# Performance work log

Measured on AMD Instinct MI355X. Metric: run time of the kernel, lower is better.

## Reference

```python
import jax, jax.numpy as jnp
import numpy as np

EMBED = 8      # embed_dim channels of 32-blade multivectors
HIDDEN = 32    # hidden_dim channels
BLADES = 32    # 2^5 Clifford blades
DT = 0.01


def setup_inputs() -> dict:
    key = jax.random.key(0)
    ks = jax.random.split(key, 8)
    B, S, N, D = 32, 256, 16, 6
    scale = lambda k, shape: jax.random.normal(k, shape, jnp.float32) * 0.1
    return {
        "x": jax.random.normal(ks[0], (B, S, N, D), jnp.float32),
        # input_proj: Linear(6, embed_dim*32)
        "W_in": scale(ks[1], (D, EMBED * BLADES)),
        "b_in": jnp.zeros((EMBED * BLADES,), jnp.float32),
        # VersorLinear(embed, hidden): channel-mixing weight shared across blades, per-blade bias
        "W1": scale(ks[2], (HIDDEN, EMBED)),
        "b1": scale(ks[3], (HIDDEN, BLADES)),
        "W2": scale(ks[4], (HIDDEN, HIDDEN)),
        "b2": scale(ks[5], (HIDDEN, BLADES)),
        "W3": scale(ks[6], (1, HIDDEN)),
        "b3": scale(ks[7], (1, BLADES)),
    }


def _versor_linear(h, W, b):
    # h: [..., in_ch, 32 blades]; mix channels, shared over blades
    return jnp.einsum('...ik,oi->...ok', h, W) + b


def _versor_act(h):
    # gate each multivector channel by sigmoid of its scalar (blade-0) part
    return h * jax.nn.sigmoid(h[..., 0:1])


def _energy(x_flat, W_in, b_in, W1, b1, W2, b2, W3, b3):
    BS, N, D = x_flat.shape
    h = x_flat @ W_in + b_in                    # [BS, N, EMBED*32]
    h = h.reshape(BS, N, EMBED, BLADES)         # [BS, N, embed, 32]
    h = _versor_act(_versor_linear(h, W1, b1))
    h = _versor_act(_versor_linear(h, W2, b2))
    h = _versor_linear(h, W3, b3)               # [BS, N, 1, 32]
    return h[..., 0].sum()                      # scalar energy


def reference(x, W_in, b_in, W1, b1, W2, b2, W3, b3):
    B, S, N, D = x.shape
    x_flat = x.reshape(B * S, N, D)
    # symplectic gradient of the Hamiltonian w.r.t. state
    grads = jax.grad(_energy)(x_flat, W_in, b_in, W1, b1, W2, b2, W3, b3)
    dq_dt = grads[..., 3:]
    dp_dt = -grads[..., :3]
    next_state = x_flat + jnp.concatenate([dq_dt, dp_dt], axis=-1) * DT
    return next_state.reshape(B, S, N, D)
```

## Files before the change

### kernel.cpp

```cpp
#include <hip/hip_runtime.h>
#include <hip/hip_bf16.h>

#define DT_STEP 0.01f

typedef __bf16 bf16x8 __attribute__((ext_vector_type(8)));
typedef float  f32x4  __attribute__((ext_vector_type(4)));

#define OFF_W2   0
#define OFF_W1   4096
#define OFF_WIND 5120
#define OFF_BIND 5312
#define OFF_B1D  5344
#define OFF_B2D  5472
#define OFF_W3   5600
#define OFF_WE   5728
#define OFF_BE   6496
#define OFF_WCP  6624
#define OFF_WAVE 7680
#define LDS_TOTAL (7680 + 4*768)

__global__ __launch_bounds__(256) void hvnn_fused(
    const float* __restrict__ x,
    const float* __restrict__ Win, const float* __restrict__ bin,
    const float* __restrict__ W1,  const float* __restrict__ b1,
    const float* __restrict__ W2,  const float* __restrict__ b2,
    const float* __restrict__ W3,
    float* __restrict__ out, int ntiles)
{
    __shared__ __align__(16) char lds[LDS_TOTAL];
    const int tid = threadIdx.x;
    const int lane = tid & 63, wv = tid >> 6;
    const int l15 = lane & 15, lhi = lane >> 4;
    const int wid = blockIdx.x * 4 + wv;
    const int nwaves = gridDim.x * 4;

    ((float4*)(lds + OFF_W2))[tid] = ((const float4*)W2)[tid];
    ((float*)(lds + OFF_W1))[tid]  = W1[tid];
    if (tid < 48) ((float*)(lds + OFF_WIND))[tid] = Win[(tid >> 3) * 256 + (tid & 7) * 32];
    if (tid < 8)  ((float*)(lds + OFF_BIND))[tid] = bin[tid * 32];
    if (tid < 32) ((float*)(lds + OFF_B1D))[tid]  = b1[tid * 32];
    if (tid < 32) ((float*)(lds + OFF_B2D))[tid]  = b2[tid * 32];
    if (tid < 32) ((float*)(lds + OFF_W3))[tid]   = W3[tid];
    __syncthreads();

    const float* W1s  = (const float*)(lds + OFF_W1);
    const float* Wind = (const float*)(lds + OFF_WIND);
    if (tid < 192) {
        int d = tid >> 5, o = tid & 31;
        float a = 0.f;
#pragma unroll
        for (int i = 0; i < 8; ++i) a = fmaf(Wind[d * 8 + i], W1s[o * 8 + i], a);
        ((float*)(lds + OFF_WE))[d * 32 + o] = a;
    }
    if (tid < 32) {
        float a = ((const float*)(lds + OFF_B1D))[tid];
#pragma unroll
        for (int i = 0; i < 8; ++i) a = fmaf(((const float*)(lds + OFF_BIND))[i], W1s[tid * 8 + i], a);
        ((float*)(lds + OFF_BE))[tid] = a;
    }
    {
        int o = tid >> 3, d = tid & 7;
        float v = 0.f;
        if (d < 6) {
            int dd = d < 3 ? d + 3 : d - 3;
            float sg = d < 3 ? DT_STEP : -DT_STEP;
            float a = 0.f;
#pragma unroll
            for (int i = 0; i < 8; ++i) a = fmaf(W1s[o * 8 + i], Wind[dd * 8 + i], a);
            v = sg * a;
        }
        ((float*)(lds + OFF_WCP))[o * 8 + d] = v;
    }
    __syncthreads();

    const float* WeS  = (const float*)(lds + OFF_WE);
    const float* W2s  = (const float*)(lds + OFF_W2);
    const float* WcpS = (const float*)(lds + OFF_WCP);
    const float* beS  = (const float*)(lds + OFF_BE);
    const float* b2dS = (const float*)(lds + OFF_B2D);
    const float* w3S  = (const float*)(lds + OFF_W3);
    const int c1 = ((l15 >> 2) << 3) | (l15 & 3);
    const int c2 = c1 + 4;

    bf16x8 awe1 = {}, awe2 = {};
    if (lhi == 0) {
#pragma unroll
        for (int d = 0; d < 6; ++d) {
            awe1[d] = (__bf16)WeS[d * 32 + c1];
            awe2[d] = (__bf16)WeS[d * 32 + c2];
        }
    }
    bf16x8 aw2f1, aw2f2, aw2b1, aw2b2;
#pragma unroll
    for (int j = 0; j < 8; ++j) {
        aw2f1[j] = (__bf16)W2s[c1 * 32 + lhi * 8 + j];
        aw2f2[j] = (__bf16)W2s[c2 * 32 + lhi * 8 + j];
        aw2b1[j] = (__bf16)W2s[(lhi * 8 + j) * 32 + c1];
        aw2b2[j] = (__bf16)W2s[(lhi * 8 + j) * 32 + c2];
    }
    bf16x8 awc = {};
    if (l15 < 6) {
#pragma unroll
        for (int j = 0; j < 8; ++j) awc[j] = (__bf16)WcpS[(lhi * 8 + j) * 8 + l15];
    }
    const f32x4 beC1 = *(const f32x4*)(beS + lhi * 8);
    const f32x4 beC2 = *(const f32x4*)(beS + lhi * 8 + 4);
    const f32x4 b2C1 = *(const f32x4*)(b2dS + lhi * 8);
    const f32x4 b2C2 = *(const f32x4*)(b2dS + lhi * 8 + 4);
    const f32x4 w3A  = *(const f32x4*)(w3S + lhi * 8);
    const f32x4 w3B  = *(const f32x4*)(w3S + lhi * 8 + 4);

    char* obufA = lds + OFF_WAVE + wv * 768;
    char* obufB = obufA + 384;
    const f32x4 z = {0.f, 0.f, 0.f, 0.f};

    auto chain = [&](bool vA, bool vB, int tA, int tB,
                     float2 xa0, float2 xa1, float2 xa2,
                     float2 xb0, float2 xb1, float2 xb2) {
        bf16x8 bxA = {}, bxB = {};
        if (lhi == 0) {
            bxA[0] = (__bf16)xa0.x; bxA[1] = (__bf16)xa0.y; bxA[2] = (__bf16)xa1.x;
            bxA[3] = (__bf16)xa1.y; bxA[4] = (__bf16)xa2.x; bxA[5] = (__bf16)xa2.y;
            bxB[0] = (__bf16)xb0.x; bxB[1] = (__bf16)xb0.y; bxB[2] = (__bf16)xb1.x;
            bxB[3] = (__bf16)xb1.y; bxB[4] = (__bf16)xb2.x; bxB[5] = (__bf16)xb2.y;
        }
        f32x4 h1A1 = __builtin_amdgcn_mfma_f32_16x16x32_bf16(awe1, bxA, beC1, 0, 0, 0);
        f32x4 h1A2 = __builtin_amdgcn_mfma_f32_16x16x32_bf16(awe2, bxA, beC2, 0, 0, 0);
        f32x4 h1B1 = __builtin_amdgcn_mfma_f32_16x16x32_bf16(awe1, bxB, beC1, 0, 0, 0);
        f32x4 h1B2 = __builtin_amdgcn_mfma_f32_16x16x32_bf16(awe2, bxB, beC2, 0, 0, 0);
        bf16x8 h1fA, h1fB; float t1A1[4], t1A2[4], t1B1[4], t1B2[4];
#pragma unroll
        for (int e = 0; e < 4; ++e) {
            float a, g;
            a = h1A1[e]; g = 1.f / (1.f + __expf(-a));
            t1A1[e] = g * fmaf(a, 1.f - g, 1.f); h1fA[e] = (__bf16)(a * g);
            a = h1A2[e]; g = 1.f / (1.f + __expf(-a));
            t1A2[e] = g * fmaf(a, 1.f - g, 1.f); h1fA[e + 4] = (__bf16)(a * g);
            a = h1B1[e]; g = 1.f / (1.f + __expf(-a));
            t1B1[e] = g * fmaf(a, 1.f - g, 1.f); h1fB[e] = (__bf16)(a * g);
            a = h1B2[e]; g = 1.f / (1.f + __expf(-a));
            t1B2[e] = g * fmaf(a, 1.f - g, 1.f); h1fB[e + 4] = (__bf16)(a * g);
        }
        f32x4 h2A1 = __builtin_amdgcn_mfma_f32_16x16x32_bf16(aw2f1, h1fA, b2C1, 0, 0, 0);
        f32x4 h2A2 = __builtin_amdgcn_mfma_f32_16x16x32_bf16(aw2f2, h1fA, b2C2, 0, 0, 0);
        f32x4 h2B1 = __builtin_amdgcn_mfma_f32_16x16x32_bf16(aw2f1, h1fB, b2C1, 0, 0, 0);
        f32x4 h2B2 = __builtin_amdgcn_mfma_f32_16x16x32_bf16(aw2f2, h1fB, b2C2, 0, 0, 0);
        bf16x8 d2fA, d2fB;
#pragma unroll
        for (int e = 0; e < 4; ++e) {
            float a, g;
            a = h2A1[e]; g = 1.f / (1.f + __expf(-a));
            d2fA[e]     = (__bf16)(w3A[e] * g * fmaf(a, 1.f - g, 1.f));
            a = h2A2[e]; g = 1.f / (1.f + __expf(-a));
            d2fA[e + 4] = (__bf16)(w3B[e] * g * fmaf(a, 1.f - g, 1.f));
            a = h2B1[e]; g = 1.f / (1.f + __expf(-a));
            d2fB[e]     = (__bf16)(w3A[e] * g * fmaf(a, 1.f - g, 1.f));
            a = h2B2[e]; g = 1.f / (1.f + __expf(-a));
            d2fB[e + 4] = (__bf16)(w3B[e] * g * fmaf(a, 1.f - g, 1.f));
        }
        f32x4 u1A1 = __builtin_amdgcn_mfma_f32_16x16x32_bf16(aw2b1, d2fA, z, 0, 0, 0);
        f32x4 u1A2 = __builtin_amdgcn_mfma_f32_16x16x32_bf16(aw2b2, d2fA, z, 0, 0, 0);
        f32x4 u1B1 = __builtin_amdgcn_mfma_f32_16x16x32_bf16(aw2b1, d2fB, z, 0, 0, 0);
        f32x4 u1B2 = __builtin_amdgcn_mfma_f32_16x16x32_bf16(aw2b2, d2fB, z, 0, 0, 0);
        bf16x8 d1fA, d1fB;
#pragma unroll
        for (int e = 0; e < 4; ++e) {
            d1fA[e]     = (__bf16)(u1A1[e] * t1A1[e]);
            d1fA[e + 4] = (__bf16)(u1A2[e] * t1A2[e]);
            d1fB[e]     = (__bf16)(u1B1[e] * t1B1[e]);
            d1fB[e + 4] = (__bf16)(u1B2[e] * t1B2[e]);
        }
        f32x4 gxA = __builtin_amdgcn_mfma_f32_16x16x32_bf16(awc, d1fA, z, 0, 0, 0);
        f32x4 gxB = __builtin_amdgcn_mfma_f32_16x16x32_bf16(awc, d1fB, z, 0, 0, 0);

        if (lhi < 2) {
#pragma unroll
            for (int e = 0; e < 4; ++e) {
                int d = lhi * 4 + e;
                if (d < 6) {
                    *(float*)(obufA + l15 * 24 + d * 4) = gxA[e];
                    *(float*)(obufB + l15 * 24 + d * 4) = gxB[e];
                }
            }
        }
        if (lane < 48) {
            if (vA) {
                float2 xv = ((const float2*)x)[(size_t)tA * 48 + lane];
                float2 g2 = *(const float2*)(obufA + lane * 8);
                ((float2*)out)[(size_t)tA * 48 + lane] = make_float2(xv.x + g2.x, xv.y + g2.y);
            }
            if (vB) {
                float2 xv = ((const float2*)x)[(size_t)tB * 48 + lane];
                float2 g2 = *(const float2*)(obufB + lane * 8);
                ((float2*)out)[(size_t)tB * 48 + lane] = make_float2(xv.x + g2.x, xv.y + g2.y);
            }
        }
    };

    const int p0 = wid, p1 = nwaves + wid;
    const int tA0 = 2 * p0, tB0 = 2 * p0 + 1, tA1 = 2 * p1, tB1 = 2 * p1 + 1;
    const bool vA0 = tA0 < ntiles, vB0 = tB0 < ntiles;
    const bool vA1 = tA1 < ntiles, vB1 = tB1 < ntiles;

    float2 a00 = {}, a01 = {}, a02 = {}, b00 = {}, b01 = {}, b02 = {};
    float2 a10 = {}, a11 = {}, a12 = {}, b10 = {}, b11 = {}, b12 = {};
    if (lhi == 0) {
        const float2* xf2 = (const float2*)x;
        if (vA0) { const float2* p = xf2 + (size_t)tA0 * 48 + l15 * 3; a00 = p[0]; a01 = p[1]; a02 = p[2]; }
        if (vB0) { const float2* p = xf2 + (size_t)tB0 * 48 + l15 * 3; b00 = p[0]; b01 = p[1]; b02 = p[2]; }
        if (vA1) { const float2* p = xf2 + (size_t)tA1 * 48 + l15 * 3; a10 = p[0]; a11 = p[1]; a12 = p[2]; }
        if (vB1) { const float2* p = xf2 + (size_t)tB1 * 48 + l15 * 3; b10 = p[0]; b11 = p[1]; b12 = p[2]; }
    }
    chain(vA0, vB0, tA0, tB0, a00, a01, a02, b00, b01, b02);
    chain(vA1, vB1, tA1, tB1, a10, a11, a12, b10, b11, b12);
}

extern "C" void kernel_launch(void* const* d_in, const int* in_sizes, int n_in,
                              void* d_out, int out_size, void* d_ws, size_t ws_size,
                              hipStream_t stream) {
    const float* x    = (const float*)d_in[0];
    const float* W_in = (const float*)d_in[1];
    const float* b_in = (const float*)d_in[2];
    const float* W1   = (const float*)d_in[3];
    const float* b1   = (const float*)d_in[4];
    const float* W2   = (const float*)d_in[5];
    const float* b2   = (const float*)d_in[6];
    const float* W3   = (const float*)d_in[7];
    float* out = (float*)d_out;

    const int NS     = in_sizes[0] / 6;
    const int ntiles = (NS + 15) / 16;
    const int blocks = (ntiles + 15) / 16;

    hvnn_fused<<<blocks, 256, 0, stream>>>(x, W_in, b_in, W1, b1, W2, b2, W3, out, ntiles);
}
```

Measured before the change: 15.38 us.

## Halve per-wave work, double grid, prefetch x early, pre-pack bf16 weights in LDS

Each wave now processes one pair of tiles instead of two, and the grid is doubled to match. This raises parallelism and shortens the serial chain each wave runs. x loads, including the residual values used in the final add, are issued at kernel start so they overlap the LDS weight setup. W2 is stored in LDS as bf16 in both row and column order, and the output projection as transposed bf16, so MFMA operands load as single vector reads instead of per-element gathers and conversions. The trade-off is twice as many blocks, each repeating the weight-setup prologue.

After: 13.72 us. 10.8% less time.

```diff
diff --git a/kernel.cpp b/kernel.cpp
--- a/kernel.cpp
+++ b/kernel.cpp
@@ -4,9 +4,11 @@
 #define DT_STEP 0.01f
 
 typedef __bf16 bf16x8 __attribute__((ext_vector_type(8)));
+typedef __bf16 bf16x4 __attribute__((ext_vector_type(4)));
 typedef float  f32x4  __attribute__((ext_vector_type(4)));
 
-#define OFF_W2   0
+#define OFF_W2R  0
+#define OFF_W2C  2048
 #define OFF_W1   4096
 #define OFF_WIND 5120
 #define OFF_BIND 5312
@@ -15,9 +17,9 @@
 #define OFF_W3   5600
 #define OFF_WE   5728
 #define OFF_BE   6496
-#define OFF_WCP  6624
-#define OFF_WAVE 7680
-#define LDS_TOTAL (7680 + 4*768)
+#define OFF_WCPT 6624
+#define OFF_WAVE 7168
+#define LDS_TOTAL (7168 + 4*768)
 
 __global__ __launch_bounds__(256) void hvnn_fused(
     const float* __restrict__ x,
@@ -32,10 +34,33 @@
     const int lane = tid & 63, wv = tid >> 6;
     const int l15 = lane & 15, lhi = lane >> 4;
     const int wid = blockIdx.x * 4 + wv;
-    const int nwaves = gridDim.x * 4;
-
-    ((float4*)(lds + OFF_W2))[tid] = ((const float4*)W2)[tid];
-    ((float*)(lds + OFF_W1))[tid]  = W1[tid];
+    const int tA = wid * 2, tB = tA + 1;
+    const bool vA = tA < ntiles, vB = tB < ntiles;
+
+    float2 xa0 = {}, xa1 = {}, xa2 = {}, xb0 = {}, xb1 = {}, xb2 = {};
+    float2 xsA = {}, xsB = {};
+    if (lhi == 0) {
+        const float2* xf2 = (const float2*)x;
+        if (vA) { const float2* p = xf2 + (size_t)tA * 48 + l15 * 3; xa0 = p[0]; xa1 = p[1]; xa2 = p[2]; }
+        if (vB) { const float2* p = xf2 + (size_t)tB * 48 + l15 * 3; xb0 = p[0]; xb1 = p[1]; xb2 = p[2]; }
+    }
+    if (lane < 48) {
+        if (vA) xsA = ((const float2*)x)[(size_t)tA * 48 + lane];
+        if (vB) xsB = ((const float2*)x)[(size_t)tB * 48 + lane];
+    }
+
+    {
+        float4 w4 = ((const float4*)W2)[tid];
+        int r = tid >> 3, c0 = (tid & 7) * 4;
+        bf16x4 b4 = { (__bf16)w4.x, (__bf16)w4.y, (__bf16)w4.z, (__bf16)w4.w };
+        *(bf16x4*)(lds + OFF_W2R + (r * 32 + c0) * 2) = b4;
+        __bf16* col = (__bf16*)(lds + OFF_W2C);
+        col[(c0 + 0) * 32 + r] = b4[0];
+        col[(c0 + 1) * 32 + r] = b4[1];
+        col[(c0 + 2) * 32 + r] = b4[2];
+        col[(c0 + 3) * 32 + r] = b4[3];
+    }
+    ((float*)(lds + OFF_W1))[tid] = W1[tid];
     if (tid < 48) ((float*)(lds + OFF_WIND))[tid] = Win[(tid >> 3) * 256 + (tid & 7) * 32];
     if (tid < 8)  ((float*)(lds + OFF_BIND))[tid] = bin[tid * 32];
     if (tid < 32) ((float*)(lds + OFF_B1D))[tid]  = b1[tid * 32];
@@ -60,28 +85,27 @@
     }
     {
         int o = tid >> 3, d = tid & 7;
-        float v = 0.f;
         if (d < 6) {
             int dd = d < 3 ? d + 3 : d - 3;
             float sg = d < 3 ? DT_STEP : -DT_STEP;
             float a = 0.f;
 #pragma unroll
             for (int i = 0; i < 8; ++i) a = fmaf(W1s[o * 8 + i], Wind[dd * 8 + i], a);
-            v = sg * a;
-        }
-        ((float*)(lds + OFF_WCP))[o * 8 + d] = v;
+            ((__bf16*)(lds + OFF_WCPT))[d * 32 + o] = (__bf16)(sg * a);
+        }
     }
     __syncthreads();
 
-    const float* WeS  = (const float*)(lds + OFF_WE);
-    const float* W2s  = (const float*)(lds + OFF_W2);
-    const float* WcpS = (const float*)(lds + OFF_WCP);
-    const float* beS  = (const float*)(lds + OFF_BE);
-    const float* b2dS = (const float*)(lds + OFF_B2D);
-    const float* w3S  = (const float*)(lds + OFF_W3);
     const int c1 = ((l15 >> 2) << 3) | (l15 & 3);
     const int c2 = c1 + 4;
-
+    const bf16x8 aw2f1 = *(const bf16x8*)(lds + OFF_W2R + (c1 * 32 + lhi * 8) * 2);
+    const bf16x8 aw2f2 = *(const bf16x8*)(lds + OFF_W2R + (c2 * 32 + lhi * 8) * 2);
+    const bf16x8 aw2b1 = *(const bf16x8*)(lds + OFF_W2C + (c1 * 32 + lhi * 8) * 2);
+    const bf16x8 aw2b2 = *(const bf16x8*)(lds + OFF_W2C + (c2 * 32 + lhi * 8) * 2);
+    bf16x8 awc = {};
+    if (l15 < 6) awc = *(const bf16x8*)(lds + OFF_WCPT + l15 * 64 + lhi * 16);
+
+    const float* WeS = (const float*)(lds + OFF_WE);
     bf16x8 awe1 = {}, awe2 = {};
     if (lhi == 0) {
 #pragma unroll
@@ -90,129 +114,100 @@
             awe2[d] = (__bf16)WeS[d * 32 + c2];
         }
     }
-    bf16x8 aw2f1, aw2f2, aw2b1, aw2b2;
-#pragma unroll
-    for (int j = 0; j < 8; ++j) {
-        aw2f1[j] = (__bf16)W2s[c1 * 32 + lhi * 8 + j];
-        aw2f2[j] = (__bf16)W2s[c2 * 32 + lhi * 8 + j];
-        aw2b1[j] = (__bf16)W2s[(lhi * 8 + j) * 32 + c1];
-        aw2b2[j] = (__bf16)W2s[(lhi * 8 + j) * 32 + c2];
-    }
-    bf16x8 awc = {};
-    if (l15 < 6) {
-#pragma unroll
-        for (int j = 0; j < 8; ++j) awc[j] = (__bf16)WcpS[(lhi * 8 + j) * 8 + l15];
-    }
-    const f32x4 beC1 = *(const f32x4*)(beS + lhi * 8);
-    const f32x4 beC2 = *(const f32x4*)(beS + lhi * 8 + 4);
-    const f32x4 b2C1 = *(const f32x4*)(b2dS + lhi * 8);
-    const f32x4 b2C2 = *(const f32x4*)(b2dS + lhi * 8 + 4);
-    const f32x4 w3A  = *(const f32x4*)(w3S + lhi * 8);
-    const f32x4 w3B  = *(const f32x4*)(w3S + lhi * 8 + 4);
+    const f32x4 beC1 = *(const f32x4*)((const float*)(lds + OFF_BE) + lhi * 8);
+    const f32x4 beC2 = *(const f32x4*)((const float*)(lds + OFF_BE) + lhi * 8 + 4);
+    const f32x4 b2C1 = *(const f32x4*)((const float*)(lds + OFF_B2D) + lhi * 8);
+    const f32x4 b2C2 = *(const f32x4*)((const float*)(lds + OFF_B2D) + lhi * 8 + 4);
+    const f32x4 w3A  = *(const f32x4*)((const float*)(lds + OFF_W3) + lhi * 8);
+    const f32x4 w3B  = *(const f32x4*)((const float*)(lds + OFF_W3) + lhi * 8 + 4);
 
     char* obufA = lds + OFF_WAVE + wv * 768;
     char* obufB = obufA + 384;
     const f32x4 z = {0.f, 0.f, 0.f, 0.f};
 
-    auto chain = [&](bool vA, bool vB, int tA, int tB,
-                     float2 xa0, float2 xa1, float2 xa2,
-                     float2 xb0, float2 xb1, float2 xb2) {
-        bf16x8 bxA = {}, bxB = {};
-        if (lhi == 0) {
-            bxA[0] = (__bf16)xa0.x; bxA[1] = (__bf16)xa0.y; bxA[2] = (__bf16)xa1.x;
-            bxA[3] = (__bf16)xa1.y; bxA[4] = (__bf16)xa2.x; bxA[5] = (__bf16)xa2.y;
-            bxB[0] = (__bf16)xb0.x; bxB[1] = (__bf16)xb0.y; bxB[2] = (__bf16)xb1.x;
-            bxB[3] = (__bf16)xb1.y; bxB[4] = (__bf16)xb2.x; bxB[5] = (__bf16)xb2.y;
-        }
-        f32x4 h1A1 = __builtin_amdgcn_mfma_f32_16x16x32_bf16(awe1, bxA, beC1, 0, 0, 0);
-        f32x4 h1A2 = __builtin_amdgcn_mfma_f32_16x16x32_bf16(awe2, bxA, beC2, 0, 0, 0);
-        f32x4 h1B1 = __builtin_amdgcn_mfma_f32_16x16x32_bf16(awe1, bxB, beC1, 0, 0, 0);
-        f32x4 h1B2 = __builtin_amdgcn_mfma_f32_16x16x32_bf16(awe2, bxB, beC2, 0, 0, 0);
-        bf16x8 h1fA, h1fB; float t1A1[4], t1A2[4], t1B1[4], t1B2[4];
+    bf16x8 bxA = {}, bxB = {};
+    if (lhi == 0) {
+        bxA[0] = (__bf16)xa0.x; bxA[1] = (__bf16)xa0.y; bxA[2] = (__bf16)xa1.x;
+        bxA[3] = (__bf16)xa1.y; bxA[4] = (__bf16)xa2.x; bxA[5] = (__bf16)xa2.y;
+        bxB[0] = (__bf16)xb0.x; bxB[1] = (__bf16)xb0.y; bxB[2] = (__bf16)xb1.x;
+        bxB[3] = (__bf16)xb1.y; bxB[4] = (__bf16)xb2.x; bxB[5] = (__bf16)xb2.y;
+    }
+
+    f32x4 h1A1 = __builtin_amdgcn_mfma_f32_16x16x32_bf16(awe1, bxA, beC1, 0, 0, 0);
+    f32x4 h1A2 = __builtin_amdgcn_mfma_f32_16x16x32_bf16(awe2, bxA, beC2, 0, 0, 0);
+    f32x4 h1B1 = __builtin_amdgcn_mfma_f32_16x16x32_bf16(awe1, bxB, beC1, 0, 0, 0);
+    f32x4 h1B2 = __builtin_amdgcn_mfma_f32_16x16x32_bf16(awe2, bxB, beC2, 0, 0, 0);
+
+    bf16x8 h1fA, h1fB; float t1A1[4], t1A2[4], t1B1[4], t1B2[4];
+#pragma unroll
+    for (int e = 0; e < 4; ++e) {
+        float a, g;
+        a = h1A1[e]; g = 1.f / (1.f + __expf(-a));
+        t1A1[e] = g * fmaf(a, 1.f - g, 1.f); h1fA[e] = (__bf16)(a * g);
+        a = h1A2[e]; g = 1.f / (1.f + __expf(-a));
+        t1A2[e] = g * fmaf(a, 1.f - g, 1.f); h1fA[e + 4] = (__bf16)(a * g);
+        a = h1B1[e]; g = 1.f / (1.f + __expf(-a));
+        t1B1[e] = g * fmaf(a, 1.f - g, 1.f); h1fB[e] = (__bf16)(a * g);
+        a = h1B2[e]; g = 1.f / (1.f + __expf(-a));
+        t1B2[e] = g * fmaf(a, 1.f - g, 1.f); h1fB[e + 4] = (__bf16)(a * g);
+    }
+
+    f32x4 h2A1 = __builtin_amdgcn_mfma_f32_16x16x32_bf16(aw2f1, h1fA, b2C1, 0, 0, 0);
+    f32x4 h2A2 = __builtin_amdgcn_mfma_f32_16x16x32_bf16(aw2f2, h1fA, b2C2, 0, 0, 0);
+    f32x4 h2B1 = __builtin_amdgcn_mfma_f32_16x16x32_bf16(aw2f1, h1fB, b2C1, 0, 0, 0);
+    f32x4 h2B2 = __builtin_amdgcn_mfma_f32_16x16x32_bf16(aw2f2, h1fB, b2C2, 0, 0, 0);
+
+    bf16x8 d2fA, d2fB;
+#pragma unroll
+    for (int e = 0; e < 4; ++e) {
+        float a, g;
+        a = h2A1[e]; g = 1.f / (1.f + __expf(-a));
+        d2fA[e]     = (__bf16)(w3A[e] * g * fmaf(a, 1.f - g, 1.f));
+        a = h2A2[e]; g = 1.f / (1.f + __expf(-a));
+        d2fA[e + 4] = (__bf16)(w3B[e] * g * fmaf(a, 1.f - g, 1.f));
+        a = h2B1[e]; g = 1.f / (1.f + __expf(-a));
+        d2fB[e]     = (__bf16)(w3A[e] * g * fmaf(a, 1.f - g, 1.f));
+        a = h2B2[e]; g = 1.f / (1.f + __expf(-a));
+        d2fB[e + 4] = (__bf16)(w3B[e] * g * fmaf(a, 1.f - g, 1.f));
+    }
+
+    f32x4 u1A1 = __builtin_amdgcn_mfma_f32_16x16x32_bf16(aw2b1, d2fA, z, 0, 0, 0);
+    f32x4 u1A2 = __builtin_amdgcn_mfma_f32_16x16x32_bf16(aw2b2, d2fA, z, 0, 0, 0);
+    f32x4 u1B1 = __builtin_amdgcn_mfma_f32_16x16x32_bf16(aw2b1, d2fB, z, 0, 0, 0);
+    f32x4 u1B2 = __builtin_amdgcn_mfma_f32_16x16x32_bf16(aw2b2, d2fB, z, 0, 0, 0);
+
+    bf16x8 d1fA, d1fB;
+#pragma unroll
+    for (int e = 0; e < 4; ++e) {
+        d1fA[e]     = (__bf16)(u1A1[e] * t1A1[e]);
+        d1fA[e + 4] = (__bf16)(u1A2[e] * t1A2[e]);
+        d1fB[e]     = (__bf16)(u1B1[e] * t1B1[e]);
+        d1fB[e + 4] = (__bf16)(u1B2[e] * t1B2[e]);
+    }
+
+    f32x4 gxA = __builtin_amdgcn_mfma_f32_16x16x32_bf16(awc, d1fA, z, 0, 0, 0);
+    f32x4 gxB = __builtin_amdgcn_mfma_f32_16x16x32_bf16(awc, d1fB, z, 0, 0, 0);
+
+    if (lhi < 2) {
 #pragma unroll
         for (int e = 0; e < 4; ++e) {
-            float a, g;
-            a = h1A1[e]; g = 1.f / (1.f + __expf(-a));
-            t1A1[e] = g * fmaf(a, 1.f - g, 1.f); h1fA[e] = (__bf16)(a * g);
-            a = h1A2[e]; g = 1.f / (1.f + __expf(-a));
-            t1A2[e] = g * fmaf(a, 1.f - g, 1.f); h1fA[e + 4] = (__bf16)(a * g);
-            a = h1B1[e]; g = 1.f / (1.f + __expf(-a));
-            t1B1[e] = g * fmaf(a, 1.f - g, 1.f); h1fB[e] = (__bf16)(a * g);
-            a = h1B2[e]; g = 1.f / (1.f + __expf(-a));
-            t1B2[e] = g * fmaf(a, 1.f - g, 1.f); h1fB[e + 4] = (__bf16)(a * g);
-        }
-        f32x4 h2A1 = __builtin_amdgcn_mfma_f32_16x16x32_bf16(aw2f1, h1fA, b2C1, 0, 0, 0);
-        f32x4 h2A2 = __builtin_amdgcn_mfma_f32_16x16x32_bf16(aw2f2, h1fA, b2C2, 0, 0, 0);
-        f32x4 h2B1 = __builtin_amdgcn_mfma_f32_16x16x32_bf16(aw2f1, h1fB, b2C1, 0, 0, 0);
-        f32x4 h2B2 = __builtin_amdgcn_mfma_f32_16x16x32_bf16(aw2f2, h1fB, b2C2, 0, 0, 0);
-        bf16x8 d2fA, d2fB;
-#pragma unroll
-        for (int e = 0; e < 4; ++e) {
-            float a, g;
-            a = h2A1[e]; g = 1.f / (1.f + __expf(-a));
-            d2fA[e]     = (__bf16)(w3A[e] * g * fmaf(a, 1.f - g, 1.f));
-            a = h2A2[e]; g = 1.f / (1.f + __expf(-a));
-            d2fA[e + 4] = (__bf16)(w3B[e] * g * fmaf(a, 1.f - g, 1.f));
-            a = h2B1[e]; g = 1.f / (1.f + __expf(-a));
-            d2fB[e]     = (__bf16)(w3A[e] * g * fmaf(a, 1.f - g, 1.f));
-            a = h2B2[e]; g = 1.f / (1.f + __expf(-a));
-            d2fB[e + 4] = (__bf16)(w3B[e] * g * fmaf(a, 1.f - g, 1.f));
-        }
-        f32x4 u1A1 = __builtin_amdgcn_mfma_f32_16x16x32_bf16(aw2b1, d2fA, z, 0, 0, 0);
-        f32x4 u1A2 = __builtin_amdgcn_mfma_f32_16x16x32_bf16(aw2b2, d2fA, z, 0, 0, 0);
-        f32x4 u1B1 = __builtin_amdgcn_mfma_f32_16x16x32_bf16(aw2b1, d2fB, z, 0, 0, 0);
-        f32x4 u1B2 = __builtin_amdgcn_mfma_f32_16x16x32_bf16(aw2b2, d2fB, z, 0, 0, 0);
-        bf16x8 d1fA, d1fB;
-#pragma unroll
-        for (int e = 0; e < 4; ++e) {
-            d1fA[e]     = (__bf16)(u1A1[e] * t1A1[e]);
-            d1fA[e + 4] = (__bf16)(u1A2[e] * t1A2[e]);
-            d1fB[e]     = (__bf16)(u1B1[e] * t1B1[e]);
-            d1fB[e + 4] = (__bf16)(u1B2[e] * t1B2[e]);
-        }
-        f32x4 gxA = __builtin_amdgcn_mfma_f32_16x16x32_bf16(awc, d1fA, z, 0, 0, 0);
-        f32x4 gxB = __builtin_amdgcn_mfma_f32_16x16x32_bf16(awc, d1fB, z, 0, 0, 0);
-
-        if (lhi < 2) {
-#pragma unroll
-            for (int e = 0; e < 4; ++e) {
-                int d = lhi * 4 + e;
-                if (d < 6) {
-                    *(float*)(obufA + l15 * 24 + d * 4) = gxA[e];
-                    *(float*)(obufB + l15 * 24 + d * 4) = gxB[e];
-                }
+            int d = lhi * 4 + e;
+            if (d < 6) {
+                *(float*)(obufA + l15 * 24 + d * 4) = gxA[e];
+                *(float*)(obufB + l15 * 24 + d * 4) = gxB[e];
             }
         }
-        if (lane < 48) {
-            if (vA) {
-                float2 xv = ((const float2*)x)[(size_t)tA * 48 + lane];
-                float2 g2 = *(const float2*)(obufA + lane * 8);
-                ((float2*)out)[(size_t)tA * 48 + lane] = make_float2(xv.x + g2.x, xv.y + g2.y);
-            }
-            if (vB) {
-                float2 xv = ((const float2*)x)[(size_t)tB * 48 + lane];
-                float2 g2 = *(const float2*)(obufB + lane * 8);
-                ((float2*)out)[(size_t)tB * 48 + lane] = make_float2(xv.x + g2.x, xv.y + g2.y);
-            }
-        }
-    };
-
-    const int p0 = wid, p1 = nwaves + wid;
-    const int tA0 = 2 * p0, tB0 = 2 * p0 + 1, tA1 = 2 * p1, tB1 = 2 * p1 + 1;
-    const bool vA0 = tA0 < ntiles, vB0 = tB0 < ntiles;
-    const bool vA1 = tA1 < ntiles, vB1 = tB1 < ntiles;
-
-    float2 a00 = {}, a01 = {}, a02 = {}, b00 = {}, b01 = {}, b02 = {};
-    float2 a10 = {}, a11 = {}, a12 = {}, b10 = {}, b11 = {}, b12 = {};
-    if (lhi == 0) {
-        const float2* xf2 = (const float2*)x;
-        if (vA0) { const float2* p = xf2 + (size_t)tA0 * 48 + l15 * 3; a00 = p[0]; a01 = p[1]; a02 = p[2]; }
-        if (vB0) { const float2* p = xf2 + (size_t)tB0 * 48 + l15 * 3; b00 = p[0]; b01 = p[1]; b02 = p[2]; }
-        if (vA1) { const float2* p = xf2 + (size_t)tA1 * 48 + l15 * 3; a10 = p[0]; a11 = p[1]; a12 = p[2]; }
-        if (vB1) { const float2* p = xf2 + (size_t)tB1 * 48 + l15 * 3; b10 = p[0]; b11 = p[1]; b12 = p[2]; }
-    }
-    chain(vA0, vB0, tA0, tB0, a00, a01, a02, b00, b01, b02);
-    chain(vA1, vB1, tA1, tB1, a10, a11, a12, b10, b11, b12);
+    }
+    if (lane < 48) {
+        if (vA) {
+            float2 g2 = *(const float2*)(obufA + lane * 8);
+            ((float2*)out)[(size_t)tA * 48 + lane] = make_float2(xsA.x + g2.x, xsA.y + g2.y);
+        }
+        if (vB) {
+            float2 g2 = *(const float2*)(obufB + lane * 8);
+            ((float2*)out)[(size_t)tB * 48 + lane] = make_float2(xsB.x + g2.x, xsB.y + g2.y);
+        }
+    }
 }
 
 extern "C" void kernel_launch(void* const* d_in, const int* in_sizes, int n_in,
@@ -230,7 +225,7 @@
 
     const int NS     = in_sizes[0] / 6;
     const int ntiles = (NS + 15) / 16;
-    const int blocks = (ntiles + 15) / 16;
+    const int blocks = (ntiles + 7) / 8;
 
     hvnn_fused<<<blocks, 256, 0, stream>>>(x, W_in, b_in, W1, b1, W2, b2, W3, out, ntiles);
 }
```
